# Kernel optimization log

Hardware: AMD Instinct MI355X
Metric: run time of the kernel (lower is better)

The kernel has to match this reference:

```python
import jax, jax.numpy as jnp
import numpy as np

N = 16777216  # number of samples
G = 16        # number of distinct group ids


def setup_inputs() -> dict:
    key = jax.random.key(0)
    k1, k2, k3, k4, k5 = jax.random.split(key, 5)
    u1 = jax.random.uniform(k1, (N,), dtype=jnp.float32)
    u2 = jax.random.uniform(k2, (N,), dtype=jnp.float32)
    u3 = jax.random.uniform(k3, (N,), dtype=jnp.float32)
    u4 = jax.random.uniform(k4, (N,), dtype=jnp.float32)
    return {
        "shape": 0.5 + 1.0 * u1,              # Weibull shape b in [0.5, 1.5]
        "scale": 0.8 + 1.2 * u2,              # Weibull scale a in [0.8, 2.0]
        "time": 0.1 + 2.9 * u3,               # survival time y in [0.1, 3.0]
        "event": (u4 > 0.5).astype(jnp.float32),  # event indicator u in {0,1}
        "lengths": jnp.arange(N, dtype=jnp.int32),   # only len(lengths)=N is used
        "group": jax.random.randint(k5, (N,), 0, G, dtype=jnp.int32),
    }


def reference(shape, scale, time, event, lengths, group):
    b, a, y, u = shape, scale, time, event
    # Per-sample Weibull NLL (torch.mean over a scalar is identity).
    hazard0 = (y + 1e-35 / a) ** b
    hazard1 = (y + 1.0 / a) ** b
    per_sample = -(u * jnp.log(jnp.exp(hazard1 - hazard0) - 1.0) - hazard1)  # [N]
    # Overall loss: sum / len(lengths) == mean over samples.
    loss = jnp.mean(per_sample)
    # Per-group mean via segment-sum (dict accumulation in the original).
    ones = jnp.ones_like(per_sample)
    counts = jax.ops.segment_sum(ones, group, num_segments=G)         # [G]
    gsum = jax.ops.segment_sum(per_sample, group, num_segments=G)     # [G]
    group_losses = gsum / jnp.maximum(counts, 1.0)                    # [G]
    return loss, group_losses
```

## Files before the change

kernel.cpp:

```cpp
#include <hip/hip_runtime.h>


namespace {
constexpr int NG = 16;
constexpr int BLOCK = 256;
constexpr float LOG2E = 1.4426950408889634f;
constexpr float LN2   = 0.6931471805599453f;
}

__device__ __forceinline__ float flog2(float x) { return __builtin_amdgcn_logf(x); }
__device__ __forceinline__ float fexp2(float x) { return __builtin_amdgcn_exp2f(x); }
__device__ __forceinline__ float frcp(float x)  { return __builtin_amdgcn_rcpf(x); }

__device__ __forceinline__ float per_sample(float b, float a, float y, float u) {
    const float inva = frcp(a);
    const float h1 = fexp2(b * flog2(y + inva));
    const float h0 = fexp2(b * flog2(y));
    const float em1 = fexp2((h1 - h0) * LOG2E) - 1.0f;
    const float t = flog2(em1) * LN2;
    return __builtin_fmaf(-u, t, h1);
}

struct Grp { float4 b, a, y, u; int4 g; };

__global__ __launch_bounds__(BLOCK, 4) void gssl_main_kernel(
    const float* __restrict__ bptr,
    const float* __restrict__ aptr,
    const float* __restrict__ yptr,
    const float* __restrict__ uptr,
    const int*   __restrict__ gptr,
    float* __restrict__ ws,
    int per_block, int n4, int n)
{
    __shared__ float sbin[2 * NG];
    const int tid = threadIdx.x;
    if (tid < 2 * NG) sbin[tid] = 0.0f;
    __syncthreads();

    float asum[NG];
    int   acnt[NG];
    #pragma unroll
    for (int q = 0; q < NG; ++q) { asum[q] = 0.0f; acnt[q] = 0; }

    const int base = blockIdx.x * per_block;
    const int rem  = n4 - base;
    const int jend = (rem < per_block) ? (rem < 0 ? 0 : rem) : per_block;

    auto ld = [&](int i) {
        Grp r;
        r.b = reinterpret_cast<const float4*>(bptr)[i];
        r.a = reinterpret_cast<const float4*>(aptr)[i];
        r.y = reinterpret_cast<const float4*>(yptr)[i];
        r.u = reinterpret_cast<const float4*>(uptr)[i];
        r.g = reinterpret_cast<const int4*>(gptr)[i];
        return r;
    };

    auto compute = [&](const Grp& G) {
        const float bb[4] = {G.b.x, G.b.y, G.b.z, G.b.w};
        const float aa[4] = {G.a.x, G.a.y, G.a.z, G.a.w};
        const float yy[4] = {G.y.x, G.y.y, G.y.z, G.y.w};
        const float uu[4] = {G.u.x, G.u.y, G.u.z, G.u.w};
        const int   gg[4] = {G.g.x, G.g.y, G.g.z, G.g.w};
        #pragma unroll
        for (int k = 0; k < 4; ++k) {
            const float ps = per_sample(bb[k], aa[k], yy[k], uu[k]);
            const int g = gg[k];
            #pragma unroll
            for (int q = 0; q < NG; ++q) {
                const bool eq = (g == q);
                asum[q] += eq ? ps : 0.0f;
                acnt[q] += (int)__popcll(__ballot(eq));
            }
        }
    };

    int j = tid;
    if (j < jend) {
        Grp cur = ld(base + j);
        for (; j + BLOCK < jend; j += BLOCK) {
            Grp nxt = ld(base + j + BLOCK);
            compute(cur);
            cur = nxt;
        }
        compute(cur);
    }

    #pragma unroll
    for (int q = 0; q < NG; ++q) {
        #pragma unroll
        for (int off = 32; off > 0; off >>= 1)
            asum[q] += __shfl_xor(asum[q], off, 64);
    }

    if ((tid & 63) == 0) {
        #pragma unroll
        for (int q = 0; q < NG; ++q) {
            atomicAdd(&sbin[q], asum[q]);
            atomicAdd(&sbin[NG + q], (float)acnt[q]);
        }
    }
    __syncthreads();

    if (tid < 2 * NG) atomicAdd(&ws[tid], sbin[tid]);

    if (blockIdx.x == 0 && tid == 0) {
        for (int i = n4 * 4; i < n; ++i) {
            const float ps = per_sample(bptr[i], aptr[i], yptr[i], uptr[i]);
            atomicAdd(&ws[gptr[i]], ps);
            atomicAdd(&ws[NG + gptr[i]], 1.0f);
        }
    }
}

__global__ __launch_bounds__(64) void gssl_final_kernel(
    const float* __restrict__ ws, float* __restrict__ out, float invN)
{
    const int t = threadIdx.x;
    if (t < NG) {
        const float gs = ws[t];
        const float gc = ws[NG + t];
        out[1 + t] = gs / fmaxf(gc, 1.0f);
    }
    float v = (t < NG) ? ws[t] : 0.0f;
    #pragma unroll
    for (int off = 32; off > 0; off >>= 1) v += __shfl_down(v, off);
    if (t == 0) out[0] = v * invN;
}

extern "C" void kernel_launch(void* const* d_in, const int* in_sizes, int n_in,
                              void* d_out, int out_size, void* d_ws, size_t ws_size,
                              hipStream_t stream) {
    const float* shape_p = (const float*)d_in[0];
    const float* scale_p = (const float*)d_in[1];
    const float* time_p  = (const float*)d_in[2];
    const float* event_p = (const float*)d_in[3];
    const int*   group_p = (const int*)d_in[5];
    float* out = (float*)d_out;
    float* ws  = (float*)d_ws;

    const int n  = in_sizes[0];
    const int n4 = n >> 2;

    hipMemsetAsync(ws, 0, 2 * NG * sizeof(float), stream);

    const int blocks = 2048;
    const int per_block = (n4 + blocks - 1) / blocks;

    hipLaunchKernelGGL(gssl_main_kernel, dim3(blocks), dim3(BLOCK), 0, stream,
                       shape_p, scale_p, time_p, event_p, group_p, ws,
                       per_block, n4, n);
    hipLaunchKernelGGL(gssl_final_kernel, dim3(1), dim3(64), 0, stream,
                       ws, out, 1.0f / (float)n);
}
```

Measured before the change: 80.34 us.

## Replace register one-hot group accumulation with per-thread padded LDS histograms

Each thread now accumulates per-group sums and counts in its own padded row of shared memory, indexed directly by the group id. This replaces the 16-way compare/select plus ballot/popcount done per sample. A strided block reduction with cross-lane shuffles and LDS atomics then combines the rows. This cuts ALU work per sample at the cost of about 35 KB of LDS per block, which may reduce occupancy, and adds LDS read-modify-write latency.

Result: faster. 73.17 us (-8.9%).

```diff
diff --git a/kernel.cpp b/kernel.cpp
--- a/kernel.cpp
+++ b/kernel.cpp
@@ -4,6 +4,7 @@
 namespace {
 constexpr int NG = 16;
 constexpr int BLOCK = 256;
+constexpr int ST = NG + 1;
 constexpr float LOG2E = 1.4426950408889634f;
 constexpr float LN2   = 0.6931471805599453f;
 }
@@ -32,15 +33,15 @@
     float* __restrict__ ws,
     int per_block, int n4, int n)
 {
+    __shared__ float lsum[BLOCK * ST];
+    __shared__ float lcnt[BLOCK * ST];
     __shared__ float sbin[2 * NG];
     const int tid = threadIdx.x;
+    const int myrow = tid * ST;
+
+    #pragma unroll
+    for (int q = 0; q < ST; ++q) { lsum[myrow + q] = 0.0f; lcnt[myrow + q] = 0.0f; }
     if (tid < 2 * NG) sbin[tid] = 0.0f;
-    __syncthreads();
-
-    float asum[NG];
-    int   acnt[NG];
-    #pragma unroll
-    for (int q = 0; q < NG; ++q) { asum[q] = 0.0f; acnt[q] = 0; }
 
     const int base = blockIdx.x * per_block;
     const int rem  = n4 - base;
@@ -56,7 +57,7 @@
         return r;
     };
 
-    auto compute = [&](const Grp& G) {
+    auto do4 = [&](const Grp& G) {
         const float bb[4] = {G.b.x, G.b.y, G.b.z, G.b.w};
         const float aa[4] = {G.a.x, G.a.y, G.a.z, G.a.w};
         const float yy[4] = {G.y.x, G.y.y, G.y.z, G.y.w};
@@ -65,13 +66,9 @@
         #pragma unroll
         for (int k = 0; k < 4; ++k) {
             const float ps = per_sample(bb[k], aa[k], yy[k], uu[k]);
-            const int g = gg[k];
-            #pragma unroll
-            for (int q = 0; q < NG; ++q) {
-                const bool eq = (g == q);
-                asum[q] += eq ? ps : 0.0f;
-                acnt[q] += (int)__popcll(__ballot(eq));
-            }
+            const int off = myrow + gg[k];
+            lsum[off] += ps;
+            lcnt[off] += 1.0f;
         }
     };
 
@@ -80,25 +77,26 @@
         Grp cur = ld(base + j);
         for (; j + BLOCK < jend; j += BLOCK) {
             Grp nxt = ld(base + j + BLOCK);
-            compute(cur);
+            do4(cur);
             cur = nxt;
         }
-        compute(cur);
+        do4(cur);
     }
+    __syncthreads();
 
+    const int q = tid & 15, c = tid >> 4;
+    float s = 0.0f, cnt = 0.0f;
     #pragma unroll
-    for (int q = 0; q < NG; ++q) {
-        #pragma unroll
-        for (int off = 32; off > 0; off >>= 1)
-            asum[q] += __shfl_xor(asum[q], off, 64);
+    for (int r = 0; r < 16; ++r) {
+        const int off = (c * 16 + r) * ST + q;
+        s   += lsum[off];
+        cnt += lcnt[off];
     }
-
-    if ((tid & 63) == 0) {
-        #pragma unroll
-        for (int q = 0; q < NG; ++q) {
-            atomicAdd(&sbin[q], asum[q]);
-            atomicAdd(&sbin[NG + q], (float)acnt[q]);
-        }
+    s   += __shfl_xor(s, 16, 64);   s   += __shfl_xor(s, 32, 64);
+    cnt += __shfl_xor(cnt, 16, 64); cnt += __shfl_xor(cnt, 32, 64);
+    if ((tid & 48) == 0) {
+        atomicAdd(&sbin[q], s);
+        atomicAdd(&sbin[NG + q], cnt);
     }
     __syncthreads();
 
```
